# Performance work log

Measured on AMD Instinct MI355X. Metric: run time of the kernel, lower is better.

The kernel has to match this reference:

```python
import jax, jax.numpy as jnp
import numpy as np

DIM = 512
HEADS = 8
DIM_HEAD = 64
DIM_INNER = HEADS * DIM_HEAD  # 512
EPS = 1e-12


def setup_inputs() -> dict:
    key = jax.random.key(0)
    ks = jax.random.split(key, 5)
    B, X, Y, N = 8, 32, 32, 1024
    fmap = jax.random.normal(ks[0], (B, DIM, X, Y), dtype=jnp.float32)
    context = jax.random.normal(ks[1], (B, N, DIM), dtype=jnp.float32)
    gamma_fmap = jnp.ones((DIM, 1, 1), dtype=jnp.float32)
    gamma_ctx = jnp.ones((DIM,), dtype=jnp.float32)
    Wq = jax.random.normal(ks[2], (DIM_INNER, DIM), dtype=jnp.float32) * 0.02
    Wkv = jax.random.normal(ks[3], (2 * DIM_INNER, DIM), dtype=jnp.float32) * 0.02
    Wout = jax.random.normal(ks[4], (DIM, DIM_INNER), dtype=jnp.float32) * 0.02
    return {"fmap": fmap, "context": context, "gamma_fmap": gamma_fmap,
            "gamma_ctx": gamma_ctx, "Wq": Wq, "Wkv": Wkv, "Wout": Wout}


def _channel_rmsnorm(x, gamma):
    # F.normalize(x, dim=1) * sqrt(dim) * gamma ; x: [b, c, x, y]
    norm = jnp.sqrt(jnp.sum(x * x, axis=1, keepdims=True))
    normed = x / jnp.maximum(norm, EPS)
    return normed * (DIM ** 0.5) * gamma


def _rmsnorm(x, gamma):
    # F.normalize(x, dim=-1) * sqrt(dim) * gamma ; x: [b, n, d]
    norm = jnp.sqrt(jnp.sum(x * x, axis=-1, keepdims=True))
    normed = x / jnp.maximum(norm, EPS)
    return normed * (DIM ** 0.5) * gamma


def reference(fmap, context, gamma_fmap, gamma_ctx, Wq, Wkv, Wout):
    B, _, X, Y = fmap.shape
    N = context.shape[1]
    H, D = HEADS, DIM_HEAD
    scale = D ** -0.5

    fm = _channel_rmsnorm(fmap, gamma_fmap)          # [b, c, x, y]
    ctx = _rmsnorm(context, gamma_ctx)               # [b, n, c]

    # 1x1 conv == channel matmul
    q = jnp.einsum('bcxy,ec->bexy', fm, Wq)          # [b, h*d, x, y]
    kv = jnp.einsum('bnc,ec->bne', ctx, Wkv)         # [b, n, 2*h*d]
    k, v = jnp.split(kv, 2, axis=-1)

    # q: b (h d) x y -> (b h) (x y) d
    q = q.reshape(B, H, D, X * Y).transpose(0, 1, 3, 2).reshape(B * H, X * Y, D)
    # k, v: b n (h d) -> (b h) n d
    k = k.reshape(B, N, H, D).transpose(0, 2, 1, 3).reshape(B * H, N, D)
    v = v.reshape(B, N, H, D).transpose(0, 2, 1, 3).reshape(B * H, N, D)

    # Euclidean cdist: sqrt(||q||^2 + ||k||^2 - 2 q.k)
    q2 = jnp.sum(q * q, axis=-1)                     # [bh, i]
    k2 = jnp.sum(k * k, axis=-1)                     # [bh, j]
    qk = jnp.einsum('bid,bjd->bij', q, k)            # [bh, i, j]
    dist = jnp.sqrt(jnp.maximum(q2[:, :, None] + k2[:, None, :] - 2.0 * qk, 0.0))
    sim = -dist * scale
    attn = jax.nn.softmax(sim, axis=-1)

    out = jnp.einsum('bij,bjd->bid', attn, v)        # [bh, xy, d]
    # (b h) (x y) d -> b (h d) x y
    out = out.reshape(B, H, X * Y, D).transpose(0, 1, 3, 2).reshape(B, H * D, X, Y)
    return jnp.einsum('bexy,de->bdxy', out, Wout)    # [b, dim, x, y]
```

## Files before the change

kernel.cpp:

```cpp
#include <hip/hip_runtime.h>
#include <math.h>

#define BATCH 8
#define CDIM 512
#define XY 1024
#define NCTX 1024
#define HEADS 8
#define DHEAD 64
#define EINNER 512
#define E2 1024

#define SQRT_DIM 22.627416997969522f

typedef short bf16x8 __attribute__((ext_vector_type(8)));
typedef float f32x4 __attribute__((ext_vector_type(4)));
typedef unsigned short ushort4v __attribute__((ext_vector_type(4)));

__device__ __forceinline__ unsigned short f2bf(float x) {
    unsigned int u = __builtin_bit_cast(unsigned int, x);
    return (unsigned short)((u + 0x7fffu + ((u >> 16) & 1u)) >> 16);
}
__device__ __forceinline__ float bf2f(unsigned short h) {
    unsigned int u = ((unsigned int)h) << 16;
    return __builtin_bit_cast(float, u);
}

__global__ __launch_bounds__(256) void k_fmap_scale(const float* __restrict__ fmap,
                                                    float* __restrict__ fscale) {
    int t = blockIdx.x * 256 + threadIdx.x;
    int b = t >> 10;
    const float* p = fmap + (size_t)b * CDIM * XY + (t & 1023);
    float ss = 0.f;
#pragma unroll 8
    for (int c = 0; c < CDIM; ++c) {
        float v = p[(size_t)c * XY];
        ss = fmaf(v, v, ss);
    }
    fscale[t] = SQRT_DIM / fmaxf(sqrtf(ss), 1e-12f);
}

__global__ __launch_bounds__(256) void k_ctx_scale(const float* __restrict__ ctx,
                                                   float* __restrict__ cscale) {
    int row = blockIdx.x * 4 + (threadIdx.x >> 6);
    int lane = threadIdx.x & 63;
    const float* p = ctx + (size_t)row * CDIM;
    float ss = 0.f;
#pragma unroll
    for (int k = 0; k < CDIM / 64; ++k) {
        float v = p[lane + 64 * k];
        ss = fmaf(v, v, ss);
    }
#pragma unroll
    for (int off = 32; off; off >>= 1) ss += __shfl_down(ss, off, 64);
    if (lane == 0) cscale[row] = SQRT_DIM / fmaxf(sqrtf(ss), 1e-12f);
}

template <bool SCALE_B>
__global__ __launch_bounds__(256) void k_gemm_nn(const float* __restrict__ A,
                                                 const float* __restrict__ Bm,
                                                 float* __restrict__ Cm,
                                                 const float* __restrict__ colscale,
                                                 const float* __restrict__ rowgamma,
                                                 int M, int N, int K) {
    const int b = blockIdx.z;
    const int n0 = blockIdx.x * 64, m0 = blockIdx.y * 64;
    const float* Bb = Bm + (size_t)b * K * N;
    float* Cb = Cm + (size_t)b * M * N;
    __shared__ float As[16][68];
    __shared__ float Bs[16][68];
    const int t = threadIdx.x;
    const int tr = t >> 4, tc = t & 15;
    const int la_k = t & 15, la_m = t >> 4;
    const int lb_n = t & 63, lb_k = t >> 6;
    float acc[4][4] = {};

    float cs = 1.f;
    if constexpr (SCALE_B) cs = colscale[(size_t)b * N + n0 + lb_n];

    for (int k0 = 0; k0 < K; k0 += 16) {
        __syncthreads();
#pragma unroll
        for (int i = 0; i < 4; ++i) {
            int m = la_m + 16 * i;
            As[la_k][m] = A[(size_t)(m0 + m) * K + k0 + la_k];
        }
#pragma unroll
        for (int i = 0; i < 4; ++i) {
            int kk = lb_k + 4 * i;
            float v = Bb[(size_t)(k0 + kk) * N + n0 + lb_n];
            if constexpr (SCALE_B) v *= cs * rowgamma[k0 + kk];
            Bs[kk][lb_n] = v;
        }
        __syncthreads();
#pragma unroll
        for (int kk = 0; kk < 16; ++kk) {
            const float4 a4 = *(const float4*)(&As[kk][tr * 4]);
            const float4 b4 = *(const float4*)(&Bs[kk][tc * 4]);
            const float ar[4] = {a4.x, a4.y, a4.z, a4.w};
            const float bc[4] = {b4.x, b4.y, b4.z, b4.w};
#pragma unroll
            for (int rr = 0; rr < 4; ++rr)
#pragma unroll
                for (int cc = 0; cc < 4; ++cc)
                    acc[rr][cc] = fmaf(ar[rr], bc[cc], acc[rr][cc]);
        }
    }
#pragma unroll
    for (int rr = 0; rr < 4; ++rr) {
        float4 v = {acc[rr][0], acc[rr][1], acc[rr][2], acc[rr][3]};
        *(float4*)(&Cb[(size_t)(m0 + tr * 4 + rr) * N + n0 + tc * 4]) = v;
    }
}

__global__ __launch_bounds__(256) void k_gemm_kv(const float* __restrict__ Am,
                                                 const float* __restrict__ Bmat,
                                                 const float* __restrict__ rowscale,
                                                 const float* __restrict__ kgamma,
                                                 unsigned short* __restrict__ khi,
                                                 unsigned short* __restrict__ klo,
                                                 unsigned short* __restrict__ vthi,
                                                 unsigned short* __restrict__ vtlo,
                                                 float* __restrict__ k2g) {
    const int b = blockIdx.z;
    const int M = NCTX, K = CDIM;
    const int n0 = blockIdx.x * 64, m0 = blockIdx.y * 64;
    const float* Ab = Am + (size_t)b * M * K;
    __shared__ float As[16][68];
    __shared__ float Bs[16][68];
    const int t = threadIdx.x;
    const int tr = t >> 4, tc = t & 15;
    const int la_k = t & 15, la_m = t >> 4;
    float acc[4][4] = {};

    float rs[4];
#pragma unroll
    for (int i = 0; i < 4; ++i)
        rs[i] = rowscale[(size_t)b * M + m0 + la_m + 16 * i];

    for (int k0 = 0; k0 < K; k0 += 16) {
        __syncthreads();
#pragma unroll
        for (int i = 0; i < 4; ++i) {
            int m = la_m + 16 * i;
            float v = Ab[(size_t)(m0 + m) * K + k0 + la_k];
            v *= rs[i] * kgamma[k0 + la_k];
            As[la_k][m] = v;
        }
#pragma unroll
        for (int i = 0; i < 4; ++i) {
            int n = la_m + 16 * i;
            Bs[la_k][n] = Bmat[(size_t)(n0 + n) * K + k0 + la_k];
        }
        __syncthreads();
#pragma unroll
        for (int kk = 0; kk < 16; ++kk) {
            const float4 a4 = *(const float4*)(&As[kk][tr * 4]);
            const float4 b4 = *(const float4*)(&Bs[kk][tc * 4]);
            const float ar[4] = {a4.x, a4.y, a4.z, a4.w};
            const float bc[4] = {b4.x, b4.y, b4.z, b4.w};
#pragma unroll
            for (int rr = 0; rr < 4; ++rr)
#pragma unroll
                for (int cc = 0; cc < 4; ++cc)
                    acc[rr][cc] = fmaf(ar[rr], bc[cc], acc[rr][cc]);
        }
    }

    const int hh = (n0 >> 6) & 7;
    const int bh_i = b * 8 + hh;
    if (n0 < EINNER) {
#pragma unroll
        for (int rr = 0; rr < 4; ++rr) {
            const int n = m0 + tr * 4 + rr;
            ushort4v h4, l4;
#pragma unroll
            for (int cc = 0; cc < 4; ++cc) {
                unsigned short h = f2bf(acc[rr][cc]);
                h4[cc] = h;
                l4[cc] = f2bf(acc[rr][cc] - bf2f(h));
            }
            *(ushort4v*)(khi + ((size_t)bh_i * NCTX + n) * 64 + tc * 4) = h4;
            *(ushort4v*)(klo + ((size_t)bh_i * NCTX + n) * 64 + tc * 4) = l4;
        }
#pragma unroll
        for (int rr = 0; rr < 4; ++rr) {
            float s = 0.f;
#pragma unroll
            for (int cc = 0; cc < 4; ++cc) s = fmaf(acc[rr][cc], acc[rr][cc], s);
            s += __shfl_xor(s, 1, 64);
            s += __shfl_xor(s, 2, 64);
            s += __shfl_xor(s, 4, 64);
            s += __shfl_xor(s, 8, 64);
            if (tc == 0) k2g[(size_t)bh_i * NCTX + m0 + tr * 4 + rr] = s;
        }
    } else {
#pragma unroll
        for (int cc = 0; cc < 4; ++cc) {
            const int d = tc * 4 + cc;
            ushort4v h4, l4;
#pragma unroll
            for (int rr = 0; rr < 4; ++rr) {
                unsigned short h = f2bf(acc[rr][cc]);
                h4[rr] = h;
                l4[rr] = f2bf(acc[rr][cc] - bf2f(h));
            }
            *(ushort4v*)(vthi + ((size_t)bh_i * 64 + d) * NCTX + m0 + tr * 4) = h4;
            *(ushort4v*)(vtlo + ((size_t)bh_i * 64 + d) * NCTX + m0 + tr * 4) = l4;
        }
    }
}

__global__ __launch_bounds__(256) void k_attn_mfma(
    const float* __restrict__ qbuf, const unsigned short* __restrict__ khi,
    const unsigned short* __restrict__ klo, const unsigned short* __restrict__ vthi,
    const unsigned short* __restrict__ vtlo, const float* __restrict__ k2g,
    float* __restrict__ ao) {
    const int bh = blockIdx.y;
    const int i0 = blockIdx.x * 64;
    const int t = threadIdx.x;
    const int w = t >> 6;
    const int lane = t & 63;
    const int c = lane & 15, g = lane >> 4;

    __shared__ __align__(16) char pool[18432];
    unsigned short* psth = (unsigned short*)(pool + w * 4608);
    unsigned short* pstl = psth + 16 * 72;
    __shared__ float q2s[64];

    const float* qb = qbuf + (size_t)bh * 64 * XY;
    const int qrow = i0 + 16 * w + c;
    float qv[16];
#pragma unroll
    for (int kk = 0; kk < 2; ++kk)
#pragma unroll
        for (int i = 0; i < 8; ++i)
            qv[kk * 8 + i] = qb[(size_t)(32 * kk + 8 * g + i) * XY + qrow];

    float s2 = 0.f;
#pragma unroll
    for (int i = 0; i < 16; ++i) s2 = fmaf(qv[i], qv[i], s2);
    s2 += __shfl_xor(s2, 16, 64);
    s2 += __shfl_xor(s2, 32, 64);
    if (g == 0) q2s[16 * w + c] = s2;
    __syncthreads();
    float q2r[4];
#pragma unroll
    for (int r = 0; r < 4; ++r) q2r[r] = q2s[16 * w + 4 * g + r];

    bf16x8 qh[2], ql[2];
#pragma unroll
    for (int kk = 0; kk < 2; ++kk)
#pragma unroll
        for (int i = 0; i < 8; ++i) {
            float x = qv[kk * 8 + i];
            unsigned short h = f2bf(x);
            qh[kk][i] = (short)h;
            ql[kk][i] = (short)f2bf(x - bf2f(h));
        }

    const unsigned short* khb = khi + (size_t)bh * NCTX * 64;
    const unsigned short* klb = klo + (size_t)bh * NCTX * 64;
    const unsigned short* vhb = vthi + (size_t)bh * 64 * NCTX;
    const unsigned short* vlb = vtlo + (size_t)bh * 64 * NCTX;
    const float* k2b = k2g + (size_t)bh * NCTX;

    f32x4 acc_o[4] = {{0.f, 0.f, 0.f, 0.f}, {0.f, 0.f, 0.f, 0.f},
                      {0.f, 0.f, 0.f, 0.f}, {0.f, 0.f, 0.f, 0.f}};
    float m_run[4], l_run[4];
#pragma unroll
    for (int r = 0; r < 4; ++r) { m_run[r] = -1e30f; l_run[r] = 0.f; }

    for (int j0 = 0; j0 < NCTX; j0 += 64) {
        float p[4][4];
#pragma unroll
        for (int cc = 0; cc < 4; ++cc) {
            const unsigned short* kr_h = khb + (size_t)(j0 + 16 * cc + c) * 64 + 8 * g;
            const unsigned short* kr_l = klb + (size_t)(j0 + 16 * cc + c) * 64 + 8 * g;
            f32x4 acc = {0.f, 0.f, 0.f, 0.f};
#pragma unroll
            for (int kk = 0; kk < 2; ++kk) {
                bf16x8 kh_ = *(const bf16x8*)(kr_h + 32 * kk);
                bf16x8 kl_ = *(const bf16x8*)(kr_l + 32 * kk);
                acc = __builtin_amdgcn_mfma_f32_16x16x32_bf16(qh[kk], kh_, acc, 0, 0, 0);
                acc = __builtin_amdgcn_mfma_f32_16x16x32_bf16(qh[kk], kl_, acc, 0, 0, 0);
                acc = __builtin_amdgcn_mfma_f32_16x16x32_bf16(ql[kk], kh_, acc, 0, 0, 0);
            }
            float k2v = k2b[j0 + 16 * cc + c];
#pragma unroll
            for (int r = 0; r < 4; ++r) {
                float d2 = q2r[r] + k2v - 2.f * acc[r];
                p[cc][r] = -0.125f * sqrtf(fmaxf(d2, 0.f));
            }
        }
        float alpha[4];
#pragma unroll
        for (int r = 0; r < 4; ++r) {
            float mt = fmaxf(fmaxf(p[0][r], p[1][r]), fmaxf(p[2][r], p[3][r]));
            mt = fmaxf(mt, __shfl_xor(mt, 1, 64));
            mt = fmaxf(mt, __shfl_xor(mt, 2, 64));
            mt = fmaxf(mt, __shfl_xor(mt, 4, 64));
            mt = fmaxf(mt, __shfl_xor(mt, 8, 64));
            float mn = fmaxf(m_run[r], mt);
            alpha[r] = __expf(m_run[r] - mn);
            m_run[r] = mn;
            float sum = 0.f;
#pragma unroll
            for (int cc = 0; cc < 4; ++cc) {
                float e = __expf(p[cc][r] - mn);
                p[cc][r] = e;
                sum += e;
            }
            sum += __shfl_xor(sum, 1, 64);
            sum += __shfl_xor(sum, 2, 64);
            sum += __shfl_xor(sum, 4, 64);
            sum += __shfl_xor(sum, 8, 64);
            l_run[r] = l_run[r] * alpha[r] + sum;
        }
#pragma unroll
        for (int dt = 0; dt < 4; ++dt)
#pragma unroll
            for (int r = 0; r < 4; ++r) acc_o[dt][r] *= alpha[r];

#pragma unroll
        for (int cc = 0; cc < 4; ++cc)
#pragma unroll
            for (int r = 0; r < 4; ++r) {
                float x = p[cc][r];
                unsigned short h = f2bf(x);
                psth[(4 * g + r) * 72 + 16 * cc + c] = h;
                pstl[(4 * g + r) * 72 + 16 * cc + c] = f2bf(x - bf2f(h));
            }
        asm volatile("s_waitcnt lgkmcnt(0)" ::: "memory");
        bf16x8 ph[2], pl[2];
#pragma unroll
        for (int kk = 0; kk < 2; ++kk) {
            ph[kk] = *(const bf16x8*)(psth + c * 72 + 32 * kk + 8 * g);
            pl[kk] = *(const bf16x8*)(pstl + c * 72 + 32 * kk + 8 * g);
        }
#pragma unroll
        for (int dt = 0; dt < 4; ++dt) {
            const unsigned short* vr_h = vhb + (size_t)(16 * dt + c) * NCTX + j0 + 8 * g;
            const unsigned short* vr_l = vlb + (size_t)(16 * dt + c) * NCTX + j0 + 8 * g;
#pragma unroll
            for (int kk = 0; kk < 2; ++kk) {
                bf16x8 vh_ = *(const bf16x8*)(vr_h + 32 * kk);
                bf16x8 vl_ = *(const bf16x8*)(vr_l + 32 * kk);
                acc_o[dt] = __builtin_amdgcn_mfma_f32_16x16x32_bf16(ph[kk], vh_, acc_o[dt], 0, 0, 0);
                acc_o[dt] = __builtin_amdgcn_mfma_f32_16x16x32_bf16(ph[kk], vl_, acc_o[dt], 0, 0, 0);
                acc_o[dt] = __builtin_amdgcn_mfma_f32_16x16x32_bf16(pl[kk], vh_, acc_o[dt], 0, 0, 0);
            }
        }
    }

    float inv[4];
#pragma unroll
    for (int r = 0; r < 4; ++r) inv[r] = 1.f / l_run[r];
    __syncthreads();
    float* tp = (float*)pool;
#pragma unroll
    for (int dt = 0; dt < 4; ++dt)
#pragma unroll
        for (int r = 0; r < 4; ++r)
            tp[(16 * w + 4 * g + r) * 68 + 16 * dt + c] = acc_o[dt][r] * inv[r];
    __syncthreads();
    const int q = t & 63;
#pragma unroll
    for (int dd = 0; dd < 16; ++dd) {
        int d = (t >> 6) * 16 + dd;
        ao[((size_t)bh * 64 + d) * XY + i0 + q] = tp[q * 68 + d];
    }
}

extern "C" void kernel_launch(void* const* d_in, const int* in_sizes, int n_in,
                              void* d_out, int out_size, void* d_ws, size_t ws_size,
                              hipStream_t stream) {
    const float* fmap    = (const float*)d_in[0];
    const float* context = (const float*)d_in[1];
    const float* gfm     = (const float*)d_in[2];
    const float* gctx    = (const float*)d_in[3];
    const float* Wq      = (const float*)d_in[4];
    const float* Wkv     = (const float*)d_in[5];
    const float* Wout    = (const float*)d_in[6];
    float* out = (float*)d_out;

    float* ws = (float*)d_ws;
    float* fscale = ws;
    float* cscale = ws + 8192;
    float* qbuf   = ws + 16384;
    float* k2g    = ws + 16384 + 4194304;
    unsigned short* khi  = (unsigned short*)(ws + 16384 + 4194304 + 65536);
    unsigned short* klo  = khi + 4194304;
    unsigned short* vthi = klo + 4194304;
    unsigned short* vtlo = vthi + 4194304;

    k_fmap_scale<<<32, 256, 0, stream>>>(fmap, fscale);
    k_ctx_scale<<<2048, 256, 0, stream>>>(context, cscale);

    k_gemm_nn<true><<<dim3(16, 8, BATCH), 256, 0, stream>>>(
        Wq, fmap, qbuf, fscale, gfm, EINNER, XY, CDIM);

    k_gemm_kv<<<dim3(16, 16, BATCH), 256, 0, stream>>>(
        context, Wkv, cscale, gctx, khi, klo, vthi, vtlo, k2g);

    k_attn_mfma<<<dim3(16, 64), 256, 0, stream>>>(
        qbuf, khi, klo, vthi, vtlo, k2g, qbuf);

    k_gemm_nn<false><<<dim3(16, 8, BATCH), 256, 0, stream>>>(
        Wout, qbuf, out, nullptr, nullptr, CDIM, XY, EINNER);
}
```

Measured before the change: 601.3 us.

## Split attention KV range across warp pairs and merge partial softmax states

Each attention block now handles 32 query rows instead of 64. Two warps share each 16-row group and each processes half of the 1024 context keys, producing partial running max, sum and output. The partials are combined through shared memory with a log-sum-exp rescale before writing. This doubles the grid to 2048 blocks to raise parallelism and shorten each warp's serial loop. The cost is that every K/V tile is loaded by twice as many blocks and an extra merge step is added.

```diff
diff --git a/kernel.cpp b/kernel.cpp
--- a/kernel.cpp
+++ b/kernel.cpp
@@ -216,19 +216,23 @@
     const unsigned short* __restrict__ vtlo, const float* __restrict__ k2g,
     float* __restrict__ ao) {
     const int bh = blockIdx.y;
-    const int i0 = blockIdx.x * 64;
+    const int i0 = blockIdx.x * 32;
     const int t = threadIdx.x;
     const int w = t >> 6;
+    const int rg = w >> 1;
+    const int jh = w & 1;
     const int lane = t & 63;
     const int c = lane & 15, g = lane >> 4;
 
     __shared__ __align__(16) char pool[18432];
     unsigned short* psth = (unsigned short*)(pool + w * 4608);
     unsigned short* pstl = psth + 16 * 72;
-    __shared__ float q2s[64];
+    __shared__ float q2s[32];
+    __shared__ float msh[4][16];
+    __shared__ float lsh[4][16];
 
     const float* qb = qbuf + (size_t)bh * 64 * XY;
-    const int qrow = i0 + 16 * w + c;
+    const int qrow = i0 + 16 * rg + c;
     float qv[16];
 #pragma unroll
     for (int kk = 0; kk < 2; ++kk)
@@ -241,11 +245,11 @@
     for (int i = 0; i < 16; ++i) s2 = fmaf(qv[i], qv[i], s2);
     s2 += __shfl_xor(s2, 16, 64);
     s2 += __shfl_xor(s2, 32, 64);
-    if (g == 0) q2s[16 * w + c] = s2;
+    if (g == 0) q2s[16 * rg + c] = s2;
     __syncthreads();
     float q2r[4];
 #pragma unroll
-    for (int r = 0; r < 4; ++r) q2r[r] = q2s[16 * w + 4 * g + r];
+    for (int r = 0; r < 4; ++r) q2r[r] = q2s[16 * rg + 4 * g + r];
 
     bf16x8 qh[2], ql[2];
 #pragma unroll
@@ -270,7 +274,8 @@
 #pragma unroll
     for (int r = 0; r < 4; ++r) { m_run[r] = -1e30f; l_run[r] = 0.f; }
 
-    for (int j0 = 0; j0 < NCTX; j0 += 64) {
+    const int jbeg = jh * 512, jend = jbeg + 512;
+    for (int j0 = jbeg; j0 < jend; j0 += 64) {
         float p[4][4];
 #pragma unroll
         for (int cc = 0; cc < 4; ++cc) {
@@ -352,22 +357,39 @@
         }
     }
 
-    float inv[4];
-#pragma unroll
-    for (int r = 0; r < 4; ++r) inv[r] = 1.f / l_run[r];
     __syncthreads();
-    float* tp = (float*)pool;
+    float* pf = (float*)pool;
 #pragma unroll
     for (int dt = 0; dt < 4; ++dt)
 #pragma unroll
         for (int r = 0; r < 4; ++r)
-            tp[(16 * w + 4 * g + r) * 68 + 16 * dt + c] = acc_o[dt][r] * inv[r];
+            pf[w * 1056 + (4 * g + r) * 66 + 16 * dt + c] = acc_o[dt][r];
+    if (c == 0) {
+#pragma unroll
+        for (int r = 0; r < 4; ++r) {
+            msh[w][4 * g + r] = m_run[r];
+            lsh[w][4 * g + r] = l_run[r];
+        }
+    }
     __syncthreads();
-    const int q = t & 63;
-#pragma unroll
-    for (int dd = 0; dd < 16; ++dd) {
-        int d = (t >> 6) * 16 + dd;
-        ao[((size_t)bh * 64 + d) * XY + i0 + q] = tp[q * 68 + d];
+
+    {
+        const int q = t & 31, dblk = t >> 5;
+        const int qrg = q >> 4, qr = q & 15;
+        const int wA = qrg * 2, wB = wA + 1;
+        float m1 = msh[wA][qr], m2 = msh[wB][qr];
+        float l1 = lsh[wA][qr], l2 = lsh[wB][qr];
+        float M = fmaxf(m1, m2);
+        float e1 = __expf(m1 - M), e2 = __expf(m2 - M);
+        float inv = 1.f / (e1 * l1 + e2 * l2);
+        float w1 = e1 * inv, w2 = e2 * inv;
+#pragma unroll
+        for (int dd = 0; dd < 8; ++dd) {
+            int d = dblk * 8 + dd;
+            float o1 = pf[wA * 1056 + qr * 66 + d];
+            float o2 = pf[wB * 1056 + qr * 66 + d];
+            ao[((size_t)bh * 64 + d) * XY + i0 + q] = w1 * o1 + w2 * o2;
+        }
     }
 }
 
@@ -402,7 +424,7 @@
     k_gemm_kv<<<dim3(16, 16, BATCH), 256, 0, stream>>>(
         context, Wkv, cscale, gctx, khi, klo, vthi, vtlo, k2g);
 
-    k_attn_mfma<<<dim3(16, 64), 256, 0, stream>>>(
+    k_attn_mfma<<<dim3(32, 64), 256, 0, stream>>>(
         qbuf, khi, klo, vthi, vtlo, k2g, qbuf);
 
     k_gemm_nn<false><<<dim3(16, 8, BATCH), 256, 0, stream>>>(
```

After: 619.0 us. +2.9%, slower.
